# Kernel tuning notes

Measured on AMD Instinct MI355X. Metric: run time of the kernel, lower is better.

Reference implementation:

```python
import jax, jax.numpy as jnp
import numpy as np

EPS = 1e-7
KERNELS = ((5, 5), (7, 1), (1, 7))
SCALES = (60, 30, 15, 8)


def avg_pool(x, kh, kw):
    # PyTorch AvgPool2d(kernel, stride=1, padding=(kh//2, kw//2)), count_include_pad=True
    s = jax.lax.reduce_window(x, 0.0, jax.lax.add, (1, 1, kh, kw), (1, 1, 1, 1),
                              ((0, 0), (0, 0), (kh // 2, kh // 2), (kw // 2, kw // 2)))
    return s / (kh * kw)


def resize_bilinear(x, oh, ow):
    # F.interpolate(mode='bilinear', align_corners=True), NCHW
    B, C, H, W = x.shape
    def coords(o, s):
        pos = jnp.arange(o) * ((s - 1) / max(o - 1, 1))
        i0 = jnp.floor(pos).astype(jnp.int32)
        i1 = jnp.minimum(i0 + 1, s - 1)
        w = (pos - i0).astype(x.dtype)
        return w, i0, i1
    wy, y0, y1 = coords(oh, H)
    wx, x0, x1 = coords(ow, W)
    rows = x[:, :, y0, :] * (1 - wy)[None, None, :, None] + x[:, :, y1, :] * wy[None, None, :, None]
    return rows[:, :, :, x0] * (1 - wx) + rows[:, :, :, x1] * wx


def setup_inputs() -> dict:
    key = jax.random.key(0)
    ks = jax.random.split(key, 12)
    B, C, H, shot = 2, 1024, 60, 1
    hid, tdim = 256, 300
    return {
        "weight": jax.random.uniform(ks[0], (B, shot, 1, 1), dtype=jnp.float32),
        "query_feat_4": jax.random.normal(ks[1], (B, C, H, H), dtype=jnp.float32),
        "supp_feats": jax.random.normal(ks[2], (shot, B, C, H, H), dtype=jnp.float32),
        "masks": jax.random.uniform(ks[3], (shot, B, 1, 473, 473), dtype=jnp.float32),
        "k": jax.random.normal(ks[4], (B, hid, H, H), dtype=jnp.float32),
        "text": jax.random.normal(ks[5], (B, tdim), dtype=jnp.float32),
        "prototype": jax.random.normal(ks[6], (B, hid, 1, 1), dtype=jnp.float32),
        "w_q": jax.random.normal(ks[7], (tdim + hid, hid), dtype=jnp.float32) * 0.05,
        "w_k": jax.random.normal(ks[8], (hid, hid), dtype=jnp.float32) * 0.05,
        "w_bl": jax.random.normal(ks[9], (hid, hid), dtype=jnp.float32) * 0.05,
        "w_proj": jax.random.normal(ks[10], (hid, hid), dtype=jnp.float32) * 0.05,
        "b_proj": jnp.zeros((hid,), dtype=jnp.float32),
    }


def reference(weight, query_feat_4, supp_feats, masks, k, text, prototype, w_q, w_k, w_bl, w_proj, b_proj):
    # ---------------- SPM: self-activation prior mask ----------------
    B, C, H, W = query_feat_4.shape
    S = H * W
    # pooled query features per kernel (shared across supports)
    q_pooled = []
    for (kh, kw) in KERNELS:
        tq = avg_pool(query_feat_4, kh, kw).reshape(B, C, S)
        tq_t = jnp.transpose(tq, (0, 2, 1))                    # [B,S,C]
        qn = jnp.sqrt((tq_t ** 2).sum(-1, keepdims=True))      # [B,S,1]
        q_pooled.append((tq_t, qn))

    corr_list = []
    for i in range(supp_feats.shape[0]):  # loop over shot (small, fixed)
        tmp_mask = resize_bilinear(masks[i], H, W)
        s = supp_feats[i] * tmp_mask
        region = []
        for (kh, kw), (tq_t, qn) in zip(KERNELS, q_pooled):
            ts = avg_pool(s, kh, kw).reshape(B, C, S)          # [B,C,S]
            sn = jnp.sqrt((ts ** 2).sum(1, keepdims=True))     # [B,1,S]
            sim = jnp.matmul(tq_t, ts) / (jnp.matmul(qn, sn) + EPS) * qn  # [B,S,S]
            sim = sim.mean(2)                                  # [B,S]
            mn = sim.min(1, keepdims=True)
            mx = sim.max(1, keepdims=True)
            sim = (sim - mn) / (mx - mn + EPS)
            region.append(sim.reshape(B, H, W))
        corr_list.append(jnp.stack(region, 1).mean(1))         # [B,H,W]
    corr = jnp.stack(corr_list, 1)                             # [B,shot,H,W]
    corr1 = (weight * corr).sum(1, keepdims=True)              # [B,1,H,W]
    corr2 = resize_bilinear(corr1, SCALES[1], SCALES[1])
    corr3 = resize_bilinear(corr1, SCALES[2], SCALES[2])
    corr4 = resize_bilinear(corr1, SCALES[3], SCALES[3])

    # ---------------- APA: bi-linear cross-modal attention ----------------
    Bk, hid, h, w = k.shape
    proto = prototype.reshape(Bk, 1, hid)                      # [B,1,hid]
    q = jnp.concatenate([text[:, None, :], proto], axis=-1)    # [B,1,embed]
    kx = jnp.einsum('oi,bihw->bohw', w_k, k).reshape(Bk, hid, h * w)
    kx = jnp.transpose(kx, (0, 2, 1))                          # [B,S,hid]
    qx = jnp.einsum('bqe,eh->bqh', q, w_q)                     # [B,1,hid]
    qw = jnp.einsum('bqh,hd->bqd', qx, w_bl)                   # bi_linear score
    score = jnp.einsum('bqd,bsd->bqs', qw, kx)                 # [B,1,S]
    score = jax.nn.softmax(score, axis=-1)
    out = jnp.einsum('bqs,bsd->bqd', score, kx)
    out = jnp.einsum('bqd,do->bqo', out, w_proj) + b_proj      # proj (dropout=eval no-op)
    out = out + proto
    return corr1, corr2, corr3, corr4, out
```

## Files before the change

kernel.cpp:

```cpp
#include <hip/hip_runtime.h>
#include <math.h>

#define EPSF 1e-7f
#define Bsz 2
#define Cch 1024
#define Hh 60
#define Ssz 3600
#define HID 256
#define TDIM 300
#define MH 473

#define TROWS 15
#define LROWS 21
#define LPITCH 68
#define CPG 8

#define OFF_PPOOL  0
#define OFF_WMAP   2764800
#define OFF_V      2786400
#define OFF_DOTP   2792544
#define OFF_NORM   3138144
#define OFF_SCORE  3159744
#define OFF_KBAR   3166944

__global__ void __launch_bounds__(256) k_pool_sn2(const float* __restrict__ supp,
                                                  const float* __restrict__ masks,
                                                  float* __restrict__ ws) {
    __shared__ float  mk[LROWS * LPITCH];
    __shared__ float2 raw[LROWS * LPITCH];
    __shared__ float2 h5s[LROWS * LPITCH];
    __shared__ float2 h7s[LROWS * LPITCH];
    int tid = threadIdx.x;
    int tile = blockIdx.x;
    int cg = blockIdx.y;
    int b = blockIdx.z;
    int y0 = tile * TROWS;

    const float2 z2 = {0.f, 0.f};
    for (int i = tid; i < LROWS * LPITCH; i += 256) {
        mk[i] = 0.f; raw[i] = z2; h5s[i] = z2; h7s[i] = z2;
    }
    __syncthreads();

    int lr[5], lx[5]; bool lv[5], la[5];
    #pragma unroll
    for (int j = 0; j < 5; ++j) {
        int idx = tid + 256 * j;
        int r = idx / 60, x = idx - 60 * r;
        lr[j] = r; lx[j] = x;
        la[j] = idx < 1260;
        int iy = y0 - 3 + r;
        lv[j] = la[j] && (iy >= 0) && (iy < Hh);
    }
    #pragma unroll
    for (int j = 0; j < 5; ++j)
        if (lv[j]) {
            int iy = y0 - 3 + lr[j];
            mk[lr[j] * LPITCH + 4 + lx[j]] =
                masks[(size_t)b * MH * MH + (size_t)(iy * 8) * MH + lx[j] * 8];
        }

    int orow[4], ox[4]; bool ov[4];
    #pragma unroll
    for (int j = 0; j < 4; ++j) {
        int o = tid + 256 * j;
        int oy = o / 60, x = o - 60 * oy;
        orow[j] = oy + 3; ox[j] = x; ov[j] = o < 900;
    }
    float a0[4] = {0,0,0,0}, a1[4] = {0,0,0,0}, a2[4] = {0,0,0,0};

    const float* chbase = supp + ((size_t)b * Cch + (size_t)cg * CPG) * Ssz + (y0 - 3) * 60;
    float pf0[5], pf1[5];
    #pragma unroll
    for (int j = 0; j < 5; ++j) {
        pf0[j] = lv[j] ? chbase[tid + 256 * j] : 0.f;
        pf1[j] = lv[j] ? chbase[Ssz + tid + 256 * j] : 0.f;
    }

    for (int p = 0; p < CPG / 2; ++p) {
        __syncthreads();
        #pragma unroll
        for (int j = 0; j < 5; ++j)
            if (lv[j]) {
                float m = mk[lr[j] * LPITCH + 4 + lx[j]];
                raw[lr[j] * LPITCH + 4 + lx[j]] = make_float2(pf0[j] * m, pf1[j] * m);
            }
        __syncthreads();
        #pragma unroll
        for (int j = 0; j < 5; ++j)
            if (la[j]) {
                int base = lr[j] * LPITCH + 4 + lx[j];
                float2 m3 = raw[base - 3], m2 = raw[base - 2], m1 = raw[base - 1];
                float2 c0 = raw[base], p1 = raw[base + 1], p2 = raw[base + 2], p3 = raw[base + 3];
                float2 h5, h7;
                h5.x = m2.x + m1.x + c0.x + p1.x + p2.x;
                h5.y = m2.y + m1.y + c0.y + p1.y + p2.y;
                h7.x = h5.x + m3.x + p3.x;
                h7.y = h5.y + m3.y + p3.y;
                h5s[base] = h5; h7s[base] = h7;
            }
        __syncthreads();
        if (p + 1 < CPG / 2) {
            const float* nb = chbase + (size_t)(2 * p + 2) * Ssz;
            #pragma unroll
            for (int j = 0; j < 5; ++j) {
                pf0[j] = lv[j] ? nb[tid + 256 * j] : 0.f;
                pf1[j] = lv[j] ? nb[Ssz + tid + 256 * j] : 0.f;
            }
        }
        #pragma unroll
        for (int j = 0; j < 4; ++j)
            if (ov[j]) {
                int base = orow[j] * LPITCH + 4 + ox[j];
                float2 sa = h5s[base - 2*LPITCH], sb = h5s[base - LPITCH], sc0 = h5s[base];
                float2 sd = h5s[base + LPITCH], se = h5s[base + 2*LPITCH];
                float p55x = (sa.x + sb.x + sc0.x + sd.x + se.x) * (1.f / 25.f);
                float p55y = (sa.y + sb.y + sc0.y + sd.y + se.y) * (1.f / 25.f);
                float2 ra = raw[base - 3*LPITCH], rb = raw[base - 2*LPITCH], rc = raw[base - LPITCH];
                float2 rd = raw[base], re = raw[base + LPITCH], rf = raw[base + 2*LPITCH], rg = raw[base + 3*LPITCH];
                float p71x = (ra.x + rb.x + rc.x + rd.x + re.x + rf.x + rg.x) * (1.f / 7.f);
                float p71y = (ra.y + rb.y + rc.y + rd.y + re.y + rf.y + rg.y) * (1.f / 7.f);
                float2 h7v = h7s[base];
                float p17x = h7v.x * (1.f / 7.f), p17y = h7v.y * (1.f / 7.f);
                a0[j] += p55x * p55x + p55y * p55y;
                a1[j] += p71x * p71x + p71y * p71y;
                a2[j] += p17x * p17x + p17y * p17y;
            }
    }
    float* dst = ws + OFF_PPOOL + (size_t)(cg * 2 + b) * 3 * Ssz;
    #pragma unroll
    for (int j = 0; j < 4; ++j)
        if (ov[j]) {
            int q = (y0 + orow[j] - 3) * 60 + ox[j];
            dst[q] = a0[j]; dst[Ssz + q] = a1[j]; dst[2 * Ssz + q] = a2[j];
        }
}

__global__ void __launch_bounds__(1024) k_wmap(const float* __restrict__ masks,
                                               float* __restrict__ ws) {
    __shared__ float inv[LROWS * LPITCH];
    int tile = blockIdx.x;
    int bk = blockIdx.y;
    int b = bk / 3, kt = bk % 3;
    int tid = threadIdx.x;
    int y0 = tile * TROWS;
    for (int i = tid; i < LROWS * LPITCH; i += 1024) inv[i] = 0.f;
    __syncthreads();
    const float* pp = ws + OFF_PPOOL + (size_t)(b * 3 + kt) * Ssz;
    #pragma unroll
    for (int j = 0; j < 2; ++j) {
        int idx = tid + 1024 * j;
        if (idx < 1260) {
            int r = idx / 60, x = idx - 60 * r;
            int iy = y0 - 3 + r;
            if (iy >= 0 && iy < Hh) {
                int q = iy * 60 + x;
                float s0 = 0.f, s1 = 0.f, s2 = 0.f, s3 = 0.f;
                #pragma unroll
                for (int g = 0; g < 128; g += 4) {
                    s0 += pp[(size_t)(g + 0) * (6 * Ssz) + q];
                    s1 += pp[(size_t)(g + 1) * (6 * Ssz) + q];
                    s2 += pp[(size_t)(g + 2) * (6 * Ssz) + q];
                    s3 += pp[(size_t)(g + 3) * (6 * Ssz) + q];
                }
                float s = (s0 + s1) + (s2 + s3);
                inv[r * LPITCH + 4 + x] = 1.0f / sqrtf(fmaxf(s, 1e-30f));
            }
        }
    }
    __syncthreads();
    int kh = (kt == 0) ? 5 : (kt == 1) ? 7 : 1;
    int kw = (kt == 0) ? 5 : (kt == 2) ? 7 : 1;
    int rh = kh / 2, rw = kw / 2;
    float norm = 1.f / (float)(kh * kw);
    int o = tid;
    if (o < 900) {
        int oy = o / 60, x = o - 60 * oy;
        int base = (oy + 3) * LPITCH + 4 + x;
        float s = 0.f;
        for (int dy = -rh; dy <= rh; ++dy)
            for (int dx = -rw; dx <= rw; ++dx)
                s += inv[base + dy * LPITCH + dx];
        int gy = y0 + oy;
        float m = masks[(size_t)b * MH * MH + (size_t)(gy * 8) * MH + x * 8];
        ws[OFF_WMAP + (size_t)bk * Ssz + gy * 60 + x] = s * norm * m;
    }
}

__global__ void k_v(const float* __restrict__ supp, float* __restrict__ ws) {
    int cB = blockIdx.x, b = blockIdx.y;
    int tid = threadIdx.x, lane = tid & 63, w = tid >> 6;
    int c0 = cB * 4;
    const float4* sp4 = (const float4*)(supp + ((size_t)b * Cch + c0) * Ssz);
    const float4* w04 = (const float4*)(ws + OFF_WMAP + (size_t)(b * 3 + 0) * Ssz);
    const float4* w14 = (const float4*)(ws + OFF_WMAP + (size_t)(b * 3 + 1) * Ssz);
    const float4* w24 = (const float4*)(ws + OFF_WMAP + (size_t)(b * 3 + 2) * Ssz);
    float a[4][3];
    #pragma unroll
    for (int cc = 0; cc < 4; ++cc) { a[cc][0] = 0; a[cc][1] = 0; a[cc][2] = 0; }
    #pragma unroll
    for (int j = 0; j < 4; ++j) {
        int idx = tid + 256 * j;
        if (idx < 900) {
            float4 g0 = w04[idx], g1 = w14[idx], g2 = w24[idx];
            #pragma unroll
            for (int cc = 0; cc < 4; ++cc) {
                float4 f = sp4[cc * 900 + idx];
                a[cc][0] += f.x * g0.x + f.y * g0.y + f.z * g0.z + f.w * g0.w;
                a[cc][1] += f.x * g1.x + f.y * g1.y + f.z * g1.z + f.w * g1.w;
                a[cc][2] += f.x * g2.x + f.y * g2.y + f.z * g2.z + f.w * g2.w;
            }
        }
    }
    #pragma unroll
    for (int m = 32; m >= 1; m >>= 1)
        #pragma unroll
        for (int cc = 0; cc < 4; ++cc) {
            a[cc][0] += __shfl_xor(a[cc][0], m, 64);
            a[cc][1] += __shfl_xor(a[cc][1], m, 64);
            a[cc][2] += __shfl_xor(a[cc][2], m, 64);
        }
    __shared__ float r[4][3][4];
    if (lane == 0)
        #pragma unroll
        for (int cc = 0; cc < 4; ++cc) {
            r[cc][0][w] = a[cc][0]; r[cc][1][w] = a[cc][1]; r[cc][2][w] = a[cc][2];
        }
    __syncthreads();
    if (tid < 12) {
        int cc = tid / 3, kk = tid - cc * 3;
        float s = r[cc][kk][0] + r[cc][kk][1] + r[cc][kk][2] + r[cc][kk][3];
        ws[OFF_V + (size_t)(b * 3 + kk) * Cch + c0 + cc] = s;
    }
}

__global__ void k_dot(const float* __restrict__ query, float* __restrict__ ws) {
    int qt = blockIdx.x, cc = blockIdx.y, b = blockIdx.z;
    int q = qt * 256 + threadIdx.x;
    if (q >= Ssz) return;
    const float* v0 = ws + OFF_V + (size_t)(b * 3 + 0) * Cch;
    const float* v1 = ws + OFF_V + (size_t)(b * 3 + 1) * Cch;
    const float* v2 = ws + OFF_V + (size_t)(b * 3 + 2) * Cch;
    float a0 = 0, a1 = 0, a2 = 0;
    int c0 = cc * 64;
    #pragma unroll 8
    for (int c = c0; c < c0 + 64; ++c) {
        float qv = query[((size_t)b * Cch + c) * Ssz + q];
        a0 += qv * v0[c]; a1 += qv * v1[c]; a2 += qv * v2[c];
    }
    float* dst = ws + OFF_DOTP + (size_t)((cc * 2 + b) * 3) * Ssz + q;
    dst[0] = a0; dst[Ssz] = a1; dst[2 * Ssz] = a2;
}

__global__ void __launch_bounds__(1024) k_sim(float* __restrict__ ws) {
    __shared__ float sA[66 * LPITCH];
    __shared__ float sB[66 * LPITCH];
    __shared__ float rmin[16], rmax[16];
    int bk = blockIdx.x; int b = bk / 3; int kt = bk % 3;
    int tid = threadIdx.x;
    int lane = tid & 63, w = tid >> 6;

    const float* dp0 = ws + OFF_DOTP + (size_t)(b * 3 + kt) * Ssz;
    for (int i = tid; i < 66 * LPITCH; i += 1024) {
        int r = i / LPITCH, col = i - r * LPITCH;
        int y = r - 3, x = col - 4;
        float s = 0.f;
        if (y >= 0 && y < Hh && x >= 0 && x < Hh) {
            int q = y * Hh + x;
            #pragma unroll
            for (int g = 0; g < 16; ++g) s += dp0[(size_t)g * 6 * Ssz + q];
        }
        sA[i] = s;
    }
    __syncthreads();
    if (kt != 1) {
        for (int idx = tid; idx < 66 * 60; idx += 1024) {
            int r = idx / 60, x = idx - 60 * r;
            int base = r * LPITCH + 4 + x;
            if (kt == 0)
                sB[base] = sA[base - 2] + sA[base - 1] + sA[base] + sA[base + 1] + sA[base + 2];
            else
                sB[base] = sA[base - 3] + sA[base - 2] + sA[base - 1] + sA[base]
                         + sA[base + 1] + sA[base + 2] + sA[base + 3];
        }
    }
    __syncthreads();
    float norm = ((kt == 0) ? (1.f / 25.f) : (1.f / 7.f)) * (1.f / (float)Ssz);
    float vals[4];
    float vmin = INFINITY, vmax = -INFINITY;
    #pragma unroll
    for (int j = 0; j < 4; ++j) {
        int q = tid + j * 1024;
        if (q < Ssz) {
            int y = q / Hh, x = q - y * Hh;
            int base = (y + 3) * LPITCH + 4 + x;
            float s;
            if (kt == 0)
                s = sB[base - 2*LPITCH] + sB[base - LPITCH] + sB[base]
                  + sB[base + LPITCH] + sB[base + 2*LPITCH];
            else if (kt == 1)
                s = sA[base - 3*LPITCH] + sA[base - 2*LPITCH] + sA[base - LPITCH]
                  + sA[base] + sA[base + LPITCH] + sA[base + 2*LPITCH] + sA[base + 3*LPITCH];
            else
                s = sB[base];
            float val = s * norm;
            vals[j] = val;
            vmin = fminf(vmin, val); vmax = fmaxf(vmax, val);
        }
    }
    #pragma unroll
    for (int m = 32; m >= 1; m >>= 1) {
        vmin = fminf(vmin, __shfl_xor(vmin, m, 64));
        vmax = fmaxf(vmax, __shfl_xor(vmax, m, 64));
    }
    if (lane == 0) { rmin[w] = vmin; rmax[w] = vmax; }
    __syncthreads();
    float mn = rmin[0], mx = rmax[0];
    #pragma unroll
    for (int ww = 1; ww < 16; ++ww) {
        mn = fminf(mn, rmin[ww]); mx = fmaxf(mx, rmax[ww]);
    }
    float inv = 1.f / (mx - mn + EPSF);
    float* np = ws + OFF_NORM + (size_t)(b * 3 + kt) * Ssz;
    #pragma unroll
    for (int j = 0; j < 4; ++j) {
        int q = tid + j * 1024;
        if (q < Ssz) np[q] = (vals[j] - mn) * inv;
    }
}

__global__ void __launch_bounds__(1024, 1)
k_apascore(const float* __restrict__ text, const float* __restrict__ proto,
           const float* __restrict__ w_q, const float* __restrict__ w_bl,
           const float* __restrict__ w_k, const float* __restrict__ kin,
           const float* __restrict__ weight, float* __restrict__ ws,
           float* __restrict__ out) {
    int st = blockIdx.x, b = blockIdx.y;
    int tid = threadIdx.x;
    int lane = tid & 63, w = tid >> 6;

    if (st == 8) {
        __shared__ float sF[Ssz];
        float wq3 = weight[b] * (1.f / 3.f);
        const float* n0 = ws + OFF_NORM + (size_t)(b * 3 + 0) * Ssz;
        const float* n1 = ws + OFF_NORM + (size_t)(b * 3 + 1) * Ssz;
        const float* n2 = ws + OFF_NORM + (size_t)(b * 3 + 2) * Ssz;
        #pragma unroll
        for (int j = 0; j < 4; ++j) {
            int q = tid + j * 1024;
            if (q < Ssz) {
                float s = n0[q] + n1[q] + n2[q];
                sF[q] = s;
                out[b * Ssz + q] = wq3 * s;
            }
        }
        __syncthreads();
        #pragma unroll
        for (int j = 0; j < 2; ++j) {
            int o = tid + j * 1024;
            if (o >= 1189) continue;
            int O, p, outi;
            if (o < 900)       { O = 30; p = o;        outi = 7200 + b * 900 + p; }
            else if (o < 1125) { O = 15; p = o - 900;  outi = 9000 + b * 225 + p; }
            else               { O = 8;  p = o - 1125; outi = 9450 + b * 64 + p; }
            int y = p / O, x = p - y * O;
            float sc = 59.f / (float)(O - 1);
            float py = y * sc, px = x * sc;
            int y0 = (int)floorf(py), x0 = (int)floorf(px);
            int y1 = min(y0 + 1, 59), x1 = min(x0 + 1, 59);
            float wy = py - y0, wx = px - x0;
            float v = sF[y0 * 60 + x0] * (1.f - wy) * (1.f - wx)
                    + sF[y1 * 60 + x0] * wy * (1.f - wx)
                    + sF[y0 * 60 + x1] * (1.f - wy) * wx
                    + sF[y1 * 60 + x1] * wy * wx;
            out[outi] = wq3 * v;
        }
        return;
    }

    __shared__ float4 p4[16][64];
    __shared__ float qxs[256], qws[256], us[256];
    const float4* wq4 = (const float4*)w_q;
    const float4* wbl4 = (const float4*)w_bl;
    const float4* wk4 = (const float4*)w_k;

    float4 acc = {0.f, 0.f, 0.f, 0.f};
    #pragma unroll
    for (int j = 0; j < 35; ++j) {
        int e = w + 16 * j;
        if (e < TDIM + HID) {
            float x = (e < TDIM) ? text[b * TDIM + e] : proto[b * HID + e - TDIM];
            float4 f = wq4[(size_t)e * 64 + lane];
            acc.x += x * f.x; acc.y += x * f.y; acc.z += x * f.z; acc.w += x * f.w;
        }
    }
    p4[w][lane] = acc;
    __syncthreads();
    if (tid < 256) {
        const float* pf = (const float*)p4;
        float s = 0.f;
        #pragma unroll
        for (int ww = 0; ww < 16; ++ww) s += pf[ww * 256 + tid];
        qxs[tid] = s;
    }
    __syncthreads();

    acc.x = acc.y = acc.z = acc.w = 0.f;
    #pragma unroll
    for (int j = 0; j < 16; ++j) {
        int e = w + 16 * j;
        float x = qxs[e];
        float4 f = wbl4[(size_t)e * 64 + lane];
        acc.x += x * f.x; acc.y += x * f.y; acc.z += x * f.z; acc.w += x * f.w;
    }
    p4[w][lane] = acc;
    __syncthreads();
    if (tid < 256) {
        const float* pf = (const float*)p4;
        float s = 0.f;
        #pragma unroll
        for (int ww = 0; ww < 16; ++ww) s += pf[ww * 256 + tid];
        qws[tid] = s;
    }
    __syncthreads();

    acc.x = acc.y = acc.z = acc.w = 0.f;
    #pragma unroll
    for (int j = 0; j < 16; ++j) {
        int e = w + 16 * j;
        float x = qws[e];
        float4 f = wk4[(size_t)e * 64 + lane];
        acc.x += x * f.x; acc.y += x * f.y; acc.z += x * f.z; acc.w += x * f.w;
    }
    p4[w][lane] = acc;
    __syncthreads();
    if (tid < 256) {
        const float* pf = (const float*)p4;
        float s = 0.f;
        #pragma unroll
        for (int ww = 0; ww < 16; ++ww) s += pf[ww * 256 + tid];
        us[tid] = s;
    }
    __syncthreads();

    if (tid < 450) {
        int s = st * 450 + tid;
        const float* kb = kin + (size_t)b * HID * Ssz + s;
        float a = 0.f;
        #pragma unroll 8
        for (int i = 0; i < HID; ++i) a += us[i] * kb[(size_t)i * Ssz];
        ws[OFF_SCORE + (size_t)b * Ssz + s] = a;
    }
}

__global__ void k_kbar(const float* __restrict__ kin, float* __restrict__ ws) {
    int i = blockIdx.x, b = blockIdx.y;
    int tid = threadIdx.x;
    int lane = tid & 63, w = tid >> 6;
    __shared__ float r1[4], r2[4];
    const float4* s4 = (const float4*)(ws + OFF_SCORE + (size_t)b * Ssz);
    float4 sv[4]; bool act[4];
    float mx = -INFINITY;
    #pragma unroll
    for (int j = 0; j < 4; ++j) {
        int idx = tid + 256 * j;
        act[j] = idx < 900;
        if (act[j]) {
            float4 v = s4[idx];
            sv[j] = v;
            mx = fmaxf(mx, fmaxf(fmaxf(v.x, v.y), fmaxf(v.z, v.w)));
        }
    }
    #pragma unroll
    for (int m = 32; m >= 1; m >>= 1) mx = fmaxf(mx, __shfl_xor(mx, m, 64));
    if (lane == 0) r1[w] = mx;
    __syncthreads();
    mx = fmaxf(fmaxf(r1[0], r1[1]), fmaxf(r1[2], r1[3]));
    __syncthreads();
    const float4* kr = (const float4*)(kin + ((size_t)b * HID + i) * Ssz);
    float se = 0.f, wsum = 0.f;
    #pragma unroll
    for (int j = 0; j < 4; ++j) {
        if (act[j]) {
            int idx = tid + 256 * j;
            float4 v = sv[j];
            float ex = expf(v.x - mx), ey = expf(v.y - mx);
            float ez = expf(v.z - mx), ew = expf(v.w - mx);
            se += ex + ey + ez + ew;
            float4 k4 = kr[idx];
            wsum += ex * k4.x + ey * k4.y + ez * k4.z + ew * k4.w;
        }
    }
    #pragma unroll
    for (int m = 32; m >= 1; m >>= 1) {
        se += __shfl_xor(se, m, 64);
        wsum += __shfl_xor(wsum, m, 64);
    }
    if (lane == 0) { r1[w] = se; r2[w] = wsum; }
    __syncthreads();
    if (tid == 0) {
        float seT = r1[0] + r1[1] + r1[2] + r1[3];
        float wsT = r2[0] + r2[1] + r2[2] + r2[3];
        ws[OFF_KBAR + b * HID + i] = wsT / seT;
    }
}

__global__ void __launch_bounds__(1024, 1)
k_apa_out(const float* __restrict__ w_k, const float* __restrict__ w_proj,
          const float* __restrict__ b_proj, const float* __restrict__ proto,
          const float* __restrict__ ws, float* __restrict__ out) {
    int b = blockIdx.x;
    int tid = threadIdx.x;
    int lane = tid & 63, w = tid >> 6;
    __shared__ float4 kbs[64];
    __shared__ float o1s[256];
    __shared__ float4 p4[16][64];
    const float4* wk4 = (const float4*)w_k;
    const float4* wp4 = (const float4*)w_proj;

    if (tid < 64) kbs[tid] = ((const float4*)(ws + OFF_KBAR + b * HID))[tid];
    __syncthreads();

    float4 kb4 = kbs[lane];
    #pragma unroll
    for (int r = 0; r < 16; ++r) {
        int h = w + 16 * r;
        float4 f = wk4[(size_t)h * 64 + lane];
        float p = f.x * kb4.x + f.y * kb4.y + f.z * kb4.z + f.w * kb4.w;
        #pragma unroll
        for (int m = 32; m >= 1; m >>= 1) p += __shfl_xor(p, m, 64);
        if (lane == 0) o1s[h] = p;
    }
    __syncthreads();

    float4 acc = {0.f, 0.f, 0.f, 0.f};
    #pragma unroll
    for (int j = 0; j < 16; ++j) {
        int d = w + 16 * j;
        float x = o1s[d];
        float4 f = wp4[(size_t)d * 64 + lane];
        acc.x += x * f.x; acc.y += x * f.y; acc.z += x * f.z; acc.w += x * f.w;
    }
    p4[w][lane] = acc;
    __syncthreads();
    if (tid < 256) {
        const float* pf = (const float*)p4;
        float s = 0.f;
        #pragma unroll
        for (int ww = 0; ww < 16; ++ww) s += pf[ww * 256 + tid];
        out[9578 + b * HID + tid] = s + b_proj[tid] + proto[b * HID + tid];
    }
}

extern "C" void kernel_launch(void* const* d_in, const int* in_sizes, int n_in,
                              void* d_out, int out_size, void* d_ws, size_t ws_size,
                              hipStream_t stream) {
    const float* weight = (const float*)d_in[0];
    const float* query  = (const float*)d_in[1];
    const float* supp   = (const float*)d_in[2];
    const float* masks  = (const float*)d_in[3];
    const float* kin    = (const float*)d_in[4];
    const float* text   = (const float*)d_in[5];
    const float* proto  = (const float*)d_in[6];
    const float* w_q    = (const float*)d_in[7];
    const float* w_k    = (const float*)d_in[8];
    const float* w_bl   = (const float*)d_in[9];
    const float* w_proj = (const float*)d_in[10];
    const float* b_proj = (const float*)d_in[11];
    float* out = (float*)d_out;
    float* ws  = (float*)d_ws;

    k_pool_sn2<<<dim3(4, 128, 2), 256, 0, stream>>>(supp, masks, ws);
    k_wmap<<<dim3(4, 6), 1024, 0, stream>>>(masks, ws);
    k_v<<<dim3(256, 2), 256, 0, stream>>>(supp, ws);
    k_dot<<<dim3(15, 16, 2), 256, 0, stream>>>(query, ws);
    k_sim<<<6, 1024, 0, stream>>>(ws);
    k_apascore<<<dim3(9, 2), 1024, 0, stream>>>(text, proto, w_q, w_bl, w_k, kin,
                                                weight, ws, out);
    k_kbar<<<dim3(HID, 2), 256, 0, stream>>>(kin, ws);
    k_apa_out<<<Bsz, 1024, 0, stream>>>(w_k, w_proj, b_proj, proto, ws, out);
}
```

Before: 216.8 us.

## Move query-vector GEMV chain into k_sim and widen score kernel parallelism

```diff
diff --git a/kernel.cpp b/kernel.cpp
--- a/kernel.cpp
+++ b/kernel.cpp
@@ -22,6 +22,7 @@
 #define OFF_NORM   3138144
 #define OFF_SCORE  3159744
 #define OFF_KBAR   3166944
+#define OFF_U      3167456
 
 __global__ void __launch_bounds__(256) k_pool_sn2(const float* __restrict__ supp,
                                                   const float* __restrict__ masks,
@@ -252,13 +253,86 @@
     dst[0] = a0; dst[Ssz] = a1; dst[2 * Ssz] = a2;
 }
 
-__global__ void __launch_bounds__(1024) k_sim(float* __restrict__ ws) {
+__global__ void __launch_bounds__(1024) k_sim(const float* __restrict__ text,
+                                              const float* __restrict__ proto,
+                                              const float* __restrict__ w_q,
+                                              const float* __restrict__ w_bl,
+                                              const float* __restrict__ w_k,
+                                              float* __restrict__ ws) {
+    int bkx = blockIdx.x;
+    int tid = threadIdx.x;
+    int lane = tid & 63, w = tid >> 6;
+
+    if (bkx >= 6) {
+        int b = bkx - 6;
+        __shared__ float4 p4[16][64];
+        __shared__ float qxs[256], qws[256];
+        const float4* wq4 = (const float4*)w_q;
+        const float4* wbl4 = (const float4*)w_bl;
+        const float4* wk4 = (const float4*)w_k;
+
+        float4 acc = {0.f, 0.f, 0.f, 0.f};
+        #pragma unroll
+        for (int j = 0; j < 35; ++j) {
+            int e = w + 16 * j;
+            if (e < TDIM + HID) {
+                float x = (e < TDIM) ? text[b * TDIM + e] : proto[b * HID + e - TDIM];
+                float4 f = wq4[(size_t)e * 64 + lane];
+                acc.x += x * f.x; acc.y += x * f.y; acc.z += x * f.z; acc.w += x * f.w;
+            }
+        }
+        p4[w][lane] = acc;
+        __syncthreads();
+        if (tid < 256) {
+            const float* pf = (const float*)p4;
+            float s = 0.f;
+            #pragma unroll
+            for (int ww = 0; ww < 16; ++ww) s += pf[ww * 256 + tid];
+            qxs[tid] = s;
+        }
+        __syncthreads();
+        acc.x = acc.y = acc.z = acc.w = 0.f;
+        #pragma unroll
+        for (int j = 0; j < 16; ++j) {
+            int e = w + 16 * j;
+            float x = qxs[e];
+            float4 f = wbl4[(size_t)e * 64 + lane];
+            acc.x += x * f.x; acc.y += x * f.y; acc.z += x * f.z; acc.w += x * f.w;
+        }
+        p4[w][lane] = acc;
+        __syncthreads();
+        if (tid < 256) {
+            const float* pf = (const float*)p4;
+            float s = 0.f;
+            #pragma unroll
+            for (int ww = 0; ww < 16; ++ww) s += pf[ww * 256 + tid];
+            qws[tid] = s;
+        }
+        __syncthreads();
+        acc.x = acc.y = acc.z = acc.w = 0.f;
+        #pragma unroll
+        for (int j = 0; j < 16; ++j) {
+            int e = w + 16 * j;
+            float x = qws[e];
+            float4 f = wk4[(size_t)e * 64 + lane];
+            acc.x += x * f.x; acc.y += x * f.y; acc.z += x * f.z; acc.w += x * f.w;
+        }
+        p4[w][lane] = acc;
+        __syncthreads();
+        if (tid < 256) {
+            const float* pf = (const float*)p4;
+            float s = 0.f;
+            #pragma unroll
+            for (int ww = 0; ww < 16; ++ww) s += pf[ww * 256 + tid];
+            ws[OFF_U + b * HID + tid] = s;
+        }
+        return;
+    }
+
     __shared__ float sA[66 * LPITCH];
     __shared__ float sB[66 * LPITCH];
     __shared__ float rmin[16], rmax[16];
-    int bk = blockIdx.x; int b = bk / 3; int kt = bk % 3;
-    int tid = threadIdx.x;
-    int lane = tid & 63, w = tid >> 6;
+    int bk = bkx; int b = bk / 3; int kt = bk % 3;
 
     const float* dp0 = ws + OFF_DOTP + (size_t)(b * 3 + kt) * Ssz;
     for (int i = tid; i < 66 * LPITCH; i += 1024) {
@@ -329,17 +403,13 @@
     }
 }
 
-__global__ void __launch_bounds__(1024, 1)
-k_apascore(const float* __restrict__ text, const float* __restrict__ proto,
-           const float* __restrict__ w_q, const float* __restrict__ w_bl,
-           const float* __restrict__ w_k, const float* __restrict__ kin,
-           const float* __restrict__ weight, float* __restrict__ ws,
-           float* __restrict__ out) {
+__global__ void __launch_bounds__(1024)
+k_score(const float* __restrict__ kin, const float* __restrict__ weight,
+        float* __restrict__ ws, float* __restrict__ out) {
     int st = blockIdx.x, b = blockIdx.y;
     int tid = threadIdx.x;
-    int lane = tid & 63, w = tid >> 6;
-
-    if (st == 8) {
+
+    if (st == 29) {
         __shared__ float sF[Ssz];
         float wq3 = weight[b] * (1.f / 3.f);
         const float* n0 = ws + OFF_NORM + (size_t)(b * 3 + 0) * Ssz;
@@ -378,78 +448,26 @@
         return;
     }
 
-    __shared__ float4 p4[16][64];
-    __shared__ float qxs[256], qws[256], us[256];
-    const float4* wq4 = (const float4*)w_q;
-    const float4* wbl4 = (const float4*)w_bl;
-    const float4* wk4 = (const float4*)w_k;
-
-    float4 acc = {0.f, 0.f, 0.f, 0.f};
-    #pragma unroll
-    for (int j = 0; j < 35; ++j) {
-        int e = w + 16 * j;
-        if (e < TDIM + HID) {
-            float x = (e < TDIM) ? text[b * TDIM + e] : proto[b * HID + e - TDIM];
-            float4 f = wq4[(size_t)e * 64 + lane];
-            acc.x += x * f.x; acc.y += x * f.y; acc.z += x * f.z; acc.w += x * f.w;
-        }
-    }
-    p4[w][lane] = acc;
-    __syncthreads();
-    if (tid < 256) {
-        const float* pf = (const float*)p4;
-        float s = 0.f;
-        #pragma unroll
-        for (int ww = 0; ww < 16; ++ww) s += pf[ww * 256 + tid];
-        qxs[tid] = s;
-    }
-    __syncthreads();
-
-    acc.x = acc.y = acc.z = acc.w = 0.f;
-    #pragma unroll
-    for (int j = 0; j < 16; ++j) {
-        int e = w + 16 * j;
-        float x = qxs[e];
-        float4 f = wbl4[(size_t)e * 64 + lane];
-        acc.x += x * f.x; acc.y += x * f.y; acc.z += x * f.z; acc.w += x * f.w;
-    }
-    p4[w][lane] = acc;
-    __syncthreads();
-    if (tid < 256) {
-        const float* pf = (const float*)p4;
-        float s = 0.f;
-        #pragma unroll
-        for (int ww = 0; ww < 16; ++ww) s += pf[ww * 256 + tid];
-        qws[tid] = s;
-    }
-    __syncthreads();
-
-    acc.x = acc.y = acc.z = acc.w = 0.f;
-    #pragma unroll
-    for (int j = 0; j < 16; ++j) {
-        int e = w + 16 * j;
-        float x = qws[e];
-        float4 f = wk4[(size_t)e * 64 + lane];
-        acc.x += x * f.x; acc.y += x * f.y; acc.z += x * f.z; acc.w += x * f.w;
-    }
-    p4[w][lane] = acc;
-    __syncthreads();
-    if (tid < 256) {
-        const float* pf = (const float*)p4;
-        float s = 0.f;
-        #pragma unroll
-        for (int ww = 0; ww < 16; ++ww) s += pf[ww * 256 + tid];
-        us[tid] = s;
-    }
-    __syncthreads();
-
-    if (tid < 450) {
-        int s = st * 450 + tid;
-        const float* kb = kin + (size_t)b * HID * Ssz + s;
-        float a = 0.f;
-        #pragma unroll 8
-        for (int i = 0; i < HID; ++i) a += us[i] * kb[(size_t)i * Ssz];
-        ws[OFF_SCORE + (size_t)b * Ssz + s] = a;
+    __shared__ float us[HID];
+    __shared__ float part[8][128];
+    if (tid < HID) us[tid] = ws[OFF_U + b * HID + tid];
+    __syncthreads();
+    int sl = tid & 127, pt = tid >> 7;
+    int s = st * 128 + sl;
+    float a = 0.f;
+    if (s < Ssz) {
+        const float* kb = kin + ((size_t)b * HID + pt * 32) * Ssz + s;
+        const float* up = us + pt * 32;
+        #pragma unroll
+        for (int i = 0; i < 32; ++i) a += up[i] * kb[(size_t)i * Ssz];
+    }
+    part[pt][sl] = a;
+    __syncthreads();
+    if (tid < 128 && st * 128 + tid < Ssz) {
+        float t = 0.f;
+        #pragma unroll
+        for (int p = 0; p < 8; ++p) t += part[p][tid];
+        ws[OFF_SCORE + (size_t)b * Ssz + st * 128 + tid] = t;
     }
 }
 
@@ -574,9 +592,8 @@
     k_wmap<<<dim3(4, 6), 1024, 0, stream>>>(masks, ws);
     k_v<<<dim3(256, 2), 256, 0, stream>>>(supp, ws);
     k_dot<<<dim3(15, 16, 2), 256, 0, stream>>>(query, ws);
-    k_sim<<<6, 1024, 0, stream>>>(ws);
-    k_apascore<<<dim3(9, 2), 1024, 0, stream>>>(text, proto, w_q, w_bl, w_k, kin,
-                                                weight, ws, out);
+    k_sim<<<8, 1024, 0, stream>>>(text, proto, w_q, w_bl, w_k, ws);
+    k_score<<<dim3(30, 2), 1024, 0, stream>>>(kin, weight, ws, out);
     k_kbar<<<dim3(HID, 2), 256, 0, stream>>>(kin, ws);
     k_apa_out<<<Bsz, 1024, 0, stream>>>(w_k, w_proj, b_proj, proto, ws, out);
 }
```

Result: faster. 205.6 us (-5.2%).
